# Performance work log

Measured on AMD Instinct MI355X. Metric: run time of the kernel, lower is better.

The kernel has to match this reference:

```python
import jax, jax.numpy as jnp
import numpy as np
from jax import lax

B, CIN, H, W = 32, 256, 28, 28
COUT, KS, KEXP = 256, 3, 4
HIDDEN = int(CIN * 0.25)  # ratio hard-coded to 0.25 in the module


def setup_inputs() -> dict:
    key = jax.random.key(0)
    k1, k2, k3, k4 = jax.random.split(key, 4)
    x = jax.random.normal(k1, (B, CIN, H, W), dtype=jnp.float32)
    # SE (InvertedEx) params: fc1 (1x1 conv, no bias), fc2 (1x1 conv, bias)
    fc1_w = jax.random.normal(k2, (HIDDEN, CIN), dtype=jnp.float32) * np.float32(np.sqrt(2.0 / CIN))
    fc2_w = jax.random.normal(k3, (KEXP * COUT, HIDDEN), dtype=jnp.float32) * np.float32(np.sqrt(2.0 / HIDDEN))
    fc2_b = jnp.zeros((KEXP * COUT,), dtype=jnp.float32)
    # K expert conv kernels, he_std = sqrt(2) * (CIN*KS^2)^-0.5
    he_std = np.float32(np.sqrt(2.0) * (CIN * KS * KS) ** -0.5)
    weight = jax.random.normal(k4, (KEXP, COUT, CIN, KS, KS), dtype=jnp.float32) * he_std
    return {"x": x, "fc1_w": fc1_w, "fc2_w": fc2_w, "fc2_b": fc2_b, "weight": weight}


def reference(x, fc1_w, fc2_w, fc2_b, weight):
    # --- SE routing ---
    pooled = jnp.mean(x, axis=(2, 3))                        # [B, CIN]
    h = jax.nn.relu(pooled @ fc1_w.T)                        # [B, HIDDEN]
    y = (h @ fc2_w.T + fc2_b).reshape(B, KEXP, COUT)         # [B, K, COUT]
    prob = jax.nn.softmax(y / jnp.sqrt(jnp.float32(HIDDEN)), axis=1)  # softmax over K
    # --- aggregate per-sample kernels ---
    agg_w = jnp.einsum('bko,koihw->boihw', prob, weight)     # [B, COUT, CIN, KS, KS]
    # --- per-sample conv (batched implicit GEMM via vmap) ---
    def conv1(xi, wi):
        return lax.conv_general_dilated(
            xi[None], wi, window_strides=(1, 1), padding=((1, 1), (1, 1)),
            dimension_numbers=('NCHW', 'OIHW', 'NCHW'))[0]
    out = jax.vmap(conv1)(x, agg_w)                          # [B, COUT, H, W]
    return out
```

## Files before the change

### kernel.cpp

```cpp
#include <hip/hip_runtime.h>
#include <math.h>

#define B_    32
#define CIN_  256
#define HW_   784
#define H_    28
#define W_    28
#define COUT_ 256
#define KEXP_ 4
#define HID_  64

typedef short short8 __attribute__((ext_vector_type(8)));
typedef unsigned short ushort4v __attribute__((ext_vector_type(4)));
typedef float floatx16 __attribute__((ext_vector_type(16)));

__device__ __forceinline__ unsigned short f2bf(float f) {
    union { float f; unsigned int u; } v; v.f = f;
    unsigned int r = (v.u + 0x7FFFu + ((v.u >> 16) & 1u)) >> 16;
    return (unsigned short)r;
}

__global__ __launch_bounds__(256) void xpose_pool_kernel(const float* __restrict__ x,
                                                         unsigned short* __restrict__ x_t,
                                                         float* __restrict__ partial) {
    __shared__ float tile[32][33];
    int bid = blockIdx.x;
    int b   = bid / 200;
    int rem = bid - b * 200;
    int icg = rem / 25;
    int pxt = rem % 25;
    int ic0 = icg * 32;
    int px0 = pxt * 32;
    int t = threadIdx.x;
    int c = t & 31, rr = t >> 5;
    #pragma unroll
    for (int r = 0; r < 4; ++r) {
        int icr = rr + r * 8;
        int px = px0 + c;
        float v = (px < HW_) ? x[((size_t)(b * CIN_ + ic0 + icr)) * HW_ + px] : 0.f;
        tile[icr][c] = v;
    }
    __syncthreads();
    #pragma unroll
    for (int r = 0; r < 4; ++r) {
        int pxr = rr + r * 8;
        int px = px0 + pxr;
        if (px < HW_)
            x_t[((size_t)b * HW_ + px) * CIN_ + ic0 + c] = f2bf(tile[c][pxr]);
    }
    if (t < 32) {
        float s = 0.f;
        #pragma unroll
        for (int cc = 0; cc < 32; ++cc) s += tile[t][cc];
        partial[((size_t)b * 25 + pxt) * CIN_ + ic0 + t] = s * (1.0f / HW_);
    }
}

__global__ __launch_bounds__(256) void pool_kernel(const float* __restrict__ x,
                                                   float* __restrict__ pooled) {
    int w = blockIdx.x * 4 + (threadIdx.x >> 6);
    int lane = threadIdx.x & 63;
    const float* p = x + (size_t)w * HW_;
    float s = 0.f;
    for (int i = lane; i < HW_; i += 64) s += p[i];
    for (int off = 32; off; off >>= 1) s += __shfl_down(s, off);
    if (lane == 0) pooled[w] = s * (1.0f / HW_);
}

__global__ __launch_bounds__(256) void se3_kernel(const float* __restrict__ partial,
                                                  const float* __restrict__ fc1_w,
                                                  const float* __restrict__ fc2_w,
                                                  const float* __restrict__ fc2_b,
                                                  float* __restrict__ prob) {
    __shared__ float pl[CIN_];
    __shared__ float h[HID_];
    __shared__ float wb[16640];
    int b = blockIdx.x, t = threadIdx.x;
    {
        float s = 0.f;
        for (int pt = 0; pt < 25; ++pt)
            s += partial[((size_t)b * 25 + pt) * CIN_ + t];
        pl[t] = s;
    }
    #pragma unroll
    for (int i = 0; i < 16; ++i) {
        int l = t + i * 256;
        float4 v = *(const float4*)(fc1_w + (size_t)l * 4);
        int r = l >> 6, cc = (l & 63) * 4;
        float* dst = &wb[r * 257 + cc];
        dst[0] = v.x; dst[1] = v.y; dst[2] = v.z; dst[3] = v.w;
    }
    __syncthreads();
    if (t < HID_) {
        float s = 0.f;
        const float* wr = &wb[t * 257];
        for (int c = 0; c < CIN_; ++c) s += pl[c] * wr[c];
        h[t] = fmaxf(s, 0.f);
    }
    float yk[KEXP_];
    for (int k = 0; k < KEXP_; ++k) {
        __syncthreads();
        #pragma unroll
        for (int i = 0; i < 16; ++i) {
            int l = t + i * 256;
            float4 v = *(const float4*)(fc2_w + (size_t)k * COUT_ * HID_ + (size_t)l * 4);
            int o = l >> 4, jj = (l & 15) * 4;
            float* dst = &wb[o * 65 + jj];
            dst[0] = v.x; dst[1] = v.y; dst[2] = v.z; dst[3] = v.w;
        }
        __syncthreads();
        float s = fc2_b[k * COUT_ + t];
        const float* wr = &wb[t * 65];
        #pragma unroll
        for (int j = 0; j < HID_; ++j) s += h[j] * wr[j];
        yk[k] = s * 0.125f;
    }
    float m = yk[0];
    for (int k = 1; k < KEXP_; ++k) m = fmaxf(m, yk[k]);
    float e[KEXP_], sum = 0.f;
    for (int k = 0; k < KEXP_; ++k) { e[k] = expf(yk[k] - m); sum += e[k]; }
    float inv = 1.0f / sum;
    for (int k = 0; k < KEXP_; ++k)
        prob[b * (KEXP_ * COUT_) + k * COUT_ + t] = e[k] * inv;
}

__global__ __launch_bounds__(256) void se2_kernel(const float* __restrict__ pooled,
                                                  const float* __restrict__ fc1_w,
                                                  const float* __restrict__ fc2_w,
                                                  const float* __restrict__ fc2_b,
                                                  float* __restrict__ prob) {
    __shared__ float pl[CIN_];
    __shared__ float h[HID_];
    __shared__ float wb[16640];
    int b = blockIdx.x, t = threadIdx.x;
    pl[t] = pooled[b * CIN_ + t];
    #pragma unroll
    for (int i = 0; i < 16; ++i) {
        int l = t + i * 256;
        float4 v = *(const float4*)(fc1_w + (size_t)l * 4);
        int r = l >> 6, cc = (l & 63) * 4;
        float* dst = &wb[r * 257 + cc];
        dst[0] = v.x; dst[1] = v.y; dst[2] = v.z; dst[3] = v.w;
    }
    __syncthreads();
    if (t < HID_) {
        float s = 0.f;
        const float* wr = &wb[t * 257];
        for (int c = 0; c < CIN_; ++c) s += pl[c] * wr[c];
        h[t] = fmaxf(s, 0.f);
    }
    float yk[KEXP_];
    for (int k = 0; k < KEXP_; ++k) {
        __syncthreads();
        #pragma unroll
        for (int i = 0; i < 16; ++i) {
            int l = t + i * 256;
            float4 v = *(const float4*)(fc2_w + (size_t)k * COUT_ * HID_ + (size_t)l * 4);
            int o = l >> 4, jj = (l & 15) * 4;
            float* dst = &wb[o * 65 + jj];
            dst[0] = v.x; dst[1] = v.y; dst[2] = v.z; dst[3] = v.w;
        }
        __syncthreads();
        float s = fc2_b[k * COUT_ + t];
        const float* wr = &wb[t * 65];
        #pragma unroll
        for (int j = 0; j < HID_; ++j) s += h[j] * wr[j];
        yk[k] = s * 0.125f;
    }
    float m = yk[0];
    for (int k = 1; k < KEXP_; ++k) m = fmaxf(m, yk[k]);
    float e[KEXP_], sum = 0.f;
    for (int k = 0; k < KEXP_; ++k) { e[k] = expf(yk[k] - m); sum += e[k]; }
    float inv = 1.0f / sum;
    for (int k = 0; k < KEXP_; ++k)
        prob[b * (KEXP_ * COUT_) + k * COUT_ + t] = e[k] * inv;
}

__global__ __launch_bounds__(256) void agg3_kernel(const float* __restrict__ weight,
                                                   const float* __restrict__ prob,
                                                   unsigned short* __restrict__ agg) {
    __shared__ float ws_w[KEXP_ * CIN_ * 9];
    __shared__ float pb[KEXP_][8];
    int bid = blockIdx.x;
    int oc = bid & 255;
    int b0 = (bid >> 8) * 8;
    int t = threadIdx.x;
    #pragma unroll
    for (int i = 0; i < 9; ++i) {
        int e4 = t + i * 256;
        int k = e4 / 576;
        int r4 = e4 - k * 576;
        float4 v = *(const float4*)(weight + (size_t)k * 589824 + (size_t)oc * 2304 + (size_t)r4 * 4);
        *(float4*)&ws_w[e4 * 4] = v;
    }
    if (t < KEXP_ * 8) {
        int k = t >> 3, bb = t & 7;
        pb[k][bb] = prob[(size_t)(b0 + bb) * (KEXP_ * COUT_) + k * COUT_ + oc];
    }
    __syncthreads();
    int icg = t & 63, blane = t >> 6;
    for (int rs = 0; rs < 9; ++rs) {
        float wv[4][4];
        #pragma unroll
        for (int q = 0; q < 4; ++q)
            #pragma unroll
            for (int k = 0; k < 4; ++k)
                wv[q][k] = ws_w[k * 2304 + (icg * 4 + q) * 9 + rs];
        #pragma unroll
        for (int bb = 0; bb < 2; ++bb) {
            int bidx = blane * 2 + bb;
            float p0 = pb[0][bidx], p1 = pb[1][bidx], p2 = pb[2][bidx], p3 = pb[3][bidx];
            ushort4v pack;
            #pragma unroll
            for (int q = 0; q < 4; ++q) {
                float s = p0 * wv[q][0] + p1 * wv[q][1] + p2 * wv[q][2] + p3 * wv[q][3];
                pack[q] = f2bf(s);
            }
            *(ushort4v*)(agg + ((((size_t)(b0 + bidx) * 9 + rs) * COUT_ + oc)) * CIN_ + icg * 4) = pack;
        }
    }
}

__global__ __launch_bounds__(256, 1) void conv_mfma3_kernel(const unsigned short* __restrict__ x_t,
                                                            const unsigned short* __restrict__ agg,
                                                            float* __restrict__ out) {
    __shared__ __align__(16) short Xs[2][9 * 35 * 72];

    int gid = blockIdx.x;
    int b      = gid & 31;
    int oc0    = ((gid >> 5) & 1) * 128;
    int rowblk = gid >> 6;
    int py0 = rowblk * 7;

    int t = threadIdx.x;
    int lane = t & 63, w = t >> 6;
    int ml = lane & 31, kh = lane >> 5;

    floatx16 acc[7];
    #pragma unroll
    for (int j = 0; j < 7; ++j)
        #pragma unroll
        for (int r = 0; r < 16; ++r) acc[j][r] = 0.f;

    const unsigned short* xtb = x_t + (size_t)b * HW_ * CIN_;
    const unsigned short* aln = agg + (((size_t)b * 9 * COUT_) + oc0 + w * 32 + ml) * CIN_ + kh * 8;

    {
        #pragma unroll
        for (int i = 0; i < 10; ++i) {
            int l = t + i * 256;
            if (l < 2520) {
                int pos = l >> 3, g = l & 7;
                int row = pos / 35, col = pos - row * 35;
                int gy = py0 - 1 + row, gx = col - 1;
                short8 v = (short8)0;
                if ((unsigned)gy < 28u && (unsigned)gx < 28u)
                    v = *(const short8*)(xtb + ((size_t)(gy * W_ + gx)) * CIN_ + g * 8);
                *(short8*)&Xs[0][pos * 72 + g * 8] = v;
            }
        }
    }

    short8 Acur0, Acur1, Acur2, Anext0, Anext1, Anext2;
    Acur0 = *(const short8*)(aln + (size_t)(0 * 3 + 0) * (COUT_ * CIN_));
    Acur1 = *(const short8*)(aln + (size_t)(1 * 3 + 0) * (COUT_ * CIN_));
    Acur2 = *(const short8*)(aln + (size_t)(2 * 3 + 0) * (COUT_ * CIN_));
    int dxn = 1, kkn = 0, icn = 0;

    __syncthreads();

    for (int c = 0; c < 4; ++c) {
        int ic0 = c * 64;
        const short* xb = &Xs[c & 1][0];

        short8 Xl[10];
        if (c < 3) {
            #pragma unroll
            for (int i = 0; i < 10; ++i) {
                int l = t + i * 256;
                short8 v = (short8)0;
                if (l < 2520) {
                    int pos = l >> 3, g = l & 7;
                    int row = pos / 35, col = pos - row * 35;
                    int gy = py0 - 1 + row, gx = col - 1;
                    if ((unsigned)gy < 28u && (unsigned)gx < 28u)
                        v = *(const short8*)(xtb + ((size_t)(gy * W_ + gx)) * CIN_ + ic0 + 64 + g * 8);
                }
                Xl[i] = v;
            }
        }

        for (int kk = 0; kk < 4; ++kk) {
            for (int dx = 0; dx < 3; ++dx) {
                if (icn < 256) {
                    const unsigned short* ap = aln + icn + kkn * 16;
                    Anext0 = *(const short8*)(ap + (size_t)(0 * 3 + dxn) * (COUT_ * CIN_));
                    Anext1 = *(const short8*)(ap + (size_t)(1 * 3 + dxn) * (COUT_ * CIN_));
                    Anext2 = *(const short8*)(ap + (size_t)(2 * 3 + dxn) * (COUT_ * CIN_));
                    ++dxn;
                    if (dxn == 3) { dxn = 0; ++kkn; if (kkn == 4) { kkn = 0; icn += 64; } }
                }
                int va = (ml + dx) * 72 + kk * 16 + kh * 8;
                #pragma unroll
                for (int r = 0; r < 9; ++r) {
                    short8 Bf = *(const short8*)&xb[r * 2520 + va];
                    if (r <= 6)
                        acc[r]     = __builtin_amdgcn_mfma_f32_32x32x16_bf16(Acur0, Bf, acc[r], 0, 0, 0);
                    if (r >= 1 && r - 1 <= 6)
                        acc[r - 1] = __builtin_amdgcn_mfma_f32_32x32x16_bf16(Acur1, Bf, acc[r - 1], 0, 0, 0);
                    if (r >= 2)
                        acc[r - 2] = __builtin_amdgcn_mfma_f32_32x32x16_bf16(Acur2, Bf, acc[r - 2], 0, 0, 0);
                }
                Acur0 = Anext0; Acur1 = Anext1; Acur2 = Anext2;
            }
        }

        if (c < 3) {
            short* dstb = &Xs[(c & 1) ^ 1][0];
            #pragma unroll
            for (int i = 0; i < 10; ++i) {
                int l = t + i * 256;
                if (l < 2520) {
                    int pos = l >> 3, g = l & 7;
                    *(short8*)&dstb[pos * 72 + g * 8] = Xl[i];
                }
            }
        }
        __syncthreads();
    }

    if (ml < W_) {
        #pragma unroll
        for (int j = 0; j < 7; ++j) {
            float* op = out + ((size_t)(b * COUT_ + oc0 + w * 32)) * HW_ + (py0 + j) * W_ + ml;
            #pragma unroll
            for (int r = 0; r < 16; ++r) {
                int ocd = (r & 3) + 8 * (r >> 2) + 4 * kh;
                op[(size_t)ocd * HW_] = acc[j][r];
            }
        }
    }
}

__global__ __launch_bounds__(256) void conv_kernel(const float* __restrict__ x,
                                                   const float* __restrict__ weight,
                                                   const float* __restrict__ prob,
                                                   float* __restrict__ out) {
    __shared__ float xs[30 * 30];
    __shared__ float wagg[8][32][12];
    __shared__ float pl[KEXP_][8];

    int b  = blockIdx.x >> 5;
    int o0 = (blockIdx.x & 31) * 8;
    int t  = threadIdx.x;

    if (t < 32) {
        int k = t >> 3, oc = t & 7;
        pl[k][oc] = prob[b * (KEXP_ * COUT_) + k * COUT_ + o0 + oc];
    }
    int p0 = t;
    int pr[4], pc[4];
    bool pv[4];
    #pragma unroll
    for (int j = 0; j < 4; ++j) {
        int p = p0 + j * 256;
        pv[j] = p < HW_;
        pr[j] = p / W_;
        pc[j] = p % W_;
    }
    float acc[8][4];
    #pragma unroll
    for (int oc = 0; oc < 8; ++oc)
        #pragma unroll
        for (int j = 0; j < 4; ++j) acc[oc][j] = 0.f;

    int aoc = t >> 5, aii = t & 31;

    for (int ic0 = 0; ic0 < CIN_; ic0 += 32) {
        __syncthreads();
        {
            float w9[9];
            #pragma unroll
            for (int j = 0; j < 9; ++j) w9[j] = 0.f;
            int i = ic0 + aii;
            #pragma unroll
            for (int k = 0; k < KEXP_; ++k) {
                float pk = pl[k][aoc];
                const float* wp = weight + ((size_t)(k * COUT_ + o0 + aoc) * CIN_ + i) * 9;
                #pragma unroll
                for (int j = 0; j < 9; ++j) w9[j] += pk * wp[j];
            }
            #pragma unroll
            for (int j = 0; j < 9; ++j) wagg[aoc][aii][j] = w9[j];
        }
        for (int ii = 0; ii < 32; ++ii) {
            int i = ic0 + ii;
            __syncthreads();
            const float* xp = x + (size_t)(b * CIN_ + i) * HW_;
            for (int e = t; e < 900; e += 256) {
                int ry = e / 30, cx = e - ry * 30;
                int gy = ry - 1, gx = cx - 1;
                float v = 0.f;
                if ((unsigned)gy < 28u && (unsigned)gx < 28u) v = xp[gy * W_ + gx];
                xs[e] = v;
            }
            __syncthreads();
            float xv[4][9];
            #pragma unroll
            for (int j = 0; j < 4; ++j) {
                if (pv[j]) {
                    const float* xr = &xs[pr[j] * 30 + pc[j]];
                    xv[j][0] = xr[0];  xv[j][1] = xr[1];  xv[j][2] = xr[2];
                    xv[j][3] = xr[30]; xv[j][4] = xr[31]; xv[j][5] = xr[32];
                    xv[j][6] = xr[60]; xv[j][7] = xr[61]; xv[j][8] = xr[62];
                } else {
                    #pragma unroll
                    for (int q = 0; q < 9; ++q) xv[j][q] = 0.f;
                }
            }
            #pragma unroll
            for (int oc = 0; oc < 8; ++oc) {
                float4 wa = *(const float4*)&wagg[oc][ii][0];
                float4 wb2 = *(const float4*)&wagg[oc][ii][4];
                float  wc = wagg[oc][ii][8];
                #pragma unroll
                for (int j = 0; j < 4; ++j) {
                    acc[oc][j] += xv[j][0] * wa.x + xv[j][1] * wa.y + xv[j][2] * wa.z
                                + xv[j][3] * wa.w + xv[j][4] * wb2.x + xv[j][5] * wb2.y
                                + xv[j][6] * wb2.z + xv[j][7] * wb2.w + xv[j][8] * wc;
                }
            }
        }
    }
    #pragma unroll
    for (int oc = 0; oc < 8; ++oc) {
        float* op = out + (size_t)(b * COUT_ + o0 + oc) * HW_ + p0;
        #pragma unroll
        for (int j = 0; j < 4; ++j)
            if (pv[j]) op[j * 256] = acc[oc][j];
    }
}

extern "C" void kernel_launch(void* const* d_in, const int* in_sizes, int n_in,
                              void* d_out, int out_size, void* d_ws, size_t ws_size,
                              hipStream_t stream) {
    const float* x     = (const float*)d_in[0];
    const float* fc1_w = (const float*)d_in[1];
    const float* fc2_w = (const float*)d_in[2];
    const float* fc2_b = (const float*)d_in[3];
    const float* weight= (const float*)d_in[4];
    float* out = (float*)d_out;

    char* ws = (char*)d_ws;
    float* prob = (float*)(ws);
    unsigned short* x_t = (unsigned short*)(ws + 131072);
    unsigned short* agg = (unsigned short*)(ws + 12976128);
    float* partial = (float*)(ws + 12976128);
    const size_t WS_NEED = 12976128 + (size_t)B_ * 9 * COUT_ * CIN_ * 2;

    if (ws_size >= WS_NEED) {
        xpose_pool_kernel<<<B_ * 8 * 25, 256, 0, stream>>>(x, x_t, partial);
        se3_kernel<<<B_, 256, 0, stream>>>(partial, fc1_w, fc2_w, fc2_b, prob);
        agg3_kernel<<<4 * COUT_, 256, 0, stream>>>(weight, prob, agg);
        conv_mfma3_kernel<<<256, 256, 0, stream>>>(x_t, agg, out);
    } else {
        float* pooled = (float*)(ws + 131072);
        pool_kernel<<<(B_ * CIN_) / 4, 256, 0, stream>>>(x, pooled);
        se2_kernel<<<B_, 256, 0, stream>>>(pooled, fc1_w, fc2_w, fc2_b, prob);
        conv_kernel<<<B_ * (COUT_ / 8), 256, 0, stream>>>(x, weight, prob, out);
    }
}
```

Baseline: 149.3 us.

## Store aggregated kernels in MFMA fragment order and retile aggregation kernel

The per-sample aggregated weights are now written in a layout matching the MFMA A-fragment order: each (batch, ic-chunk, kk, rs, oc-group) block is 512 contiguous bf16 values, so each lane's short8 load in the conv kernel is contiguous across the wave instead of strided by CIN. The aggregation kernel is retiled to 256 blocks, each covering 32 output channels, 16 input channels and 16 batches. Each block stages its weight slice in padded LDS and writes 16-byte packed stores. This targets uncoalesced A-operand global loads in the conv and the scattered small stores in aggregation, at the cost of fewer aggregation blocks and a more complex index mapping.

```diff
diff --git a/kernel.cpp b/kernel.cpp
--- a/kernel.cpp
+++ b/kernel.cpp
@@ -12,6 +12,7 @@
 
 typedef short short8 __attribute__((ext_vector_type(8)));
 typedef unsigned short ushort4v __attribute__((ext_vector_type(4)));
+typedef unsigned short ushort8v __attribute__((ext_vector_type(8)));
 typedef float floatx16 __attribute__((ext_vector_type(16)));
 
 __device__ __forceinline__ unsigned short f2bf(float f) {
@@ -176,47 +177,63 @@
         prob[b * (KEXP_ * COUT_) + k * COUT_ + t] = e[k] * inv;
 }
 
-__global__ __launch_bounds__(256) void agg3_kernel(const float* __restrict__ weight,
+__global__ __launch_bounds__(256) void agg4_kernel(const float* __restrict__ weight,
                                                    const float* __restrict__ prob,
                                                    unsigned short* __restrict__ agg) {
-    __shared__ float ws_w[KEXP_ * CIN_ * 9];
-    __shared__ float pb[KEXP_][8];
-    int bid = blockIdx.x;
-    int oc = bid & 255;
-    int b0 = (bid >> 8) * 8;
+    __shared__ float wlds[4][32][145];
+    int gid = blockIdx.x;
+    int og  = gid & 7;
+    int icc = (gid >> 3) & 3;
+    int kk  = (gid >> 5) & 3;
+    int bh  = gid >> 7;
+    int oc0 = og * 32;
+    int ic0 = icc * 64 + kk * 16;
     int t = threadIdx.x;
-    #pragma unroll
-    for (int i = 0; i < 9; ++i) {
-        int e4 = t + i * 256;
-        int k = e4 / 576;
-        int r4 = e4 - k * 576;
-        float4 v = *(const float4*)(weight + (size_t)k * 589824 + (size_t)oc * 2304 + (size_t)r4 * 4);
-        *(float4*)&ws_w[e4 * 4] = v;
-    }
-    if (t < KEXP_ * 8) {
-        int k = t >> 3, bb = t & 7;
-        pb[k][bb] = prob[(size_t)(b0 + bb) * (KEXP_ * COUT_) + k * COUT_ + oc];
+
+    #pragma unroll
+    for (int i = 0; i < 18; ++i) {
+        int idx = t + i * 256;
+        int k  = idx / 1152;
+        int r  = idx - k * 1152;
+        int oc = r / 36;
+        int f4 = r - oc * 36;
+        float4 v = *(const float4*)(weight + ((size_t)(k * COUT_ + oc0 + oc) * CIN_ + ic0) * 9 + f4 * 4);
+        float* dst = &wlds[k][oc][f4 * 4];
+        dst[0] = v.x; dst[1] = v.y; dst[2] = v.z; dst[3] = v.w;
+    }
+
+    int lane = t & 63, wv = t >> 6;
+    int ml = lane & 31, kh = lane >> 5;
+
+    float pbr[4][4];
+    #pragma unroll
+    for (int bi = 0; bi < 4; ++bi) {
+        int b = bh * 16 + wv * 4 + bi;
+        #pragma unroll
+        for (int k = 0; k < 4; ++k)
+            pbr[bi][k] = prob[(size_t)b * (KEXP_ * COUT_) + k * COUT_ + oc0 + ml];
     }
     __syncthreads();
-    int icg = t & 63, blane = t >> 6;
+
     for (int rs = 0; rs < 9; ++rs) {
-        float wv[4][4];
-        #pragma unroll
-        for (int q = 0; q < 4; ++q)
-            #pragma unroll
-            for (int k = 0; k < 4; ++k)
-                wv[q][k] = ws_w[k * 2304 + (icg * 4 + q) * 9 + rs];
-        #pragma unroll
-        for (int bb = 0; bb < 2; ++bb) {
-            int bidx = blane * 2 + bb;
-            float p0 = pb[0][bidx], p1 = pb[1][bidx], p2 = pb[2][bidx], p3 = pb[3][bidx];
-            ushort4v pack;
-            #pragma unroll
-            for (int q = 0; q < 4; ++q) {
-                float s = p0 * wv[q][0] + p1 * wv[q][1] + p2 * wv[q][2] + p3 * wv[q][3];
-                pack[q] = f2bf(s);
-            }
-            *(ushort4v*)(agg + ((((size_t)(b0 + bidx) * 9 + rs) * COUT_ + oc)) * CIN_ + icg * 4) = pack;
+        float wreg[4][8];
+        #pragma unroll
+        for (int k = 0; k < 4; ++k)
+            #pragma unroll
+            for (int j = 0; j < 8; ++j)
+                wreg[k][j] = wlds[k][ml][(kh * 8 + j) * 9 + rs];
+        #pragma unroll
+        for (int bi = 0; bi < 4; ++bi) {
+            int b = bh * 16 + wv * 4 + bi;
+            ushort8v pack;
+            #pragma unroll
+            for (int j = 0; j < 8; ++j) {
+                float s = pbr[bi][0] * wreg[0][j] + pbr[bi][1] * wreg[1][j]
+                        + pbr[bi][2] * wreg[2][j] + pbr[bi][3] * wreg[3][j];
+                pack[j] = f2bf(s);
+            }
+            *(ushort8v*)(agg + (size_t)(b * 16 + icc * 4 + kk) * 36864
+                             + (size_t)rs * 4096 + og * 512 + lane * 8) = pack;
         }
     }
 }
@@ -228,13 +245,15 @@
 
     int gid = blockIdx.x;
     int b      = gid & 31;
-    int oc0    = ((gid >> 5) & 1) * 128;
+    int half   = (gid >> 5) & 1;
+    int oc0    = half * 128;
     int rowblk = gid >> 6;
     int py0 = rowblk * 7;
 
     int t = threadIdx.x;
     int lane = t & 63, w = t >> 6;
     int ml = lane & 31, kh = lane >> 5;
+    int og = half * 4 + w;
 
     floatx16 acc[7];
     #pragma unroll
@@ -243,7 +262,7 @@
         for (int r = 0; r < 16; ++r) acc[j][r] = 0.f;
 
     const unsigned short* xtb = x_t + (size_t)b * HW_ * CIN_;
-    const unsigned short* aln = agg + (((size_t)b * 9 * COUT_) + oc0 + w * 32 + ml) * CIN_ + kh * 8;
+    const unsigned short* aln = agg + (size_t)b * 589824 + og * 512 + lane * 8;
 
     {
         #pragma unroll
@@ -262,9 +281,9 @@
     }
 
     short8 Acur0, Acur1, Acur2, Anext0, Anext1, Anext2;
-    Acur0 = *(const short8*)(aln + (size_t)(0 * 3 + 0) * (COUT_ * CIN_));
-    Acur1 = *(const short8*)(aln + (size_t)(1 * 3 + 0) * (COUT_ * CIN_));
-    Acur2 = *(const short8*)(aln + (size_t)(2 * 3 + 0) * (COUT_ * CIN_));
+    Acur0 = *(const short8*)(aln);
+    Acur1 = *(const short8*)(aln + 12288);
+    Acur2 = *(const short8*)(aln + 24576);
     int dxn = 1, kkn = 0, icn = 0;
 
     __syncthreads();
@@ -293,10 +312,11 @@
         for (int kk = 0; kk < 4; ++kk) {
             for (int dx = 0; dx < 3; ++dx) {
                 if (icn < 256) {
-                    const unsigned short* ap = aln + icn + kkn * 16;
-                    Anext0 = *(const short8*)(ap + (size_t)(0 * 3 + dxn) * (COUT_ * CIN_));
-                    Anext1 = *(const short8*)(ap + (size_t)(1 * 3 + dxn) * (COUT_ * CIN_));
-                    Anext2 = *(const short8*)(ap + (size_t)(2 * 3 + dxn) * (COUT_ * CIN_));
+                    const unsigned short* ap = aln + (size_t)(icn >> 6) * 147456
+                                                   + (size_t)kkn * 36864 + (size_t)dxn * 4096;
+                    Anext0 = *(const short8*)(ap);
+                    Anext1 = *(const short8*)(ap + 12288);
+                    Anext2 = *(const short8*)(ap + 24576);
                     ++dxn;
                     if (dxn == 3) { dxn = 0; ++kkn; if (kkn == 4) { kkn = 0; icn += 64; } }
                 }
@@ -461,7 +481,7 @@
     if (ws_size >= WS_NEED) {
         xpose_pool_kernel<<<B_ * 8 * 25, 256, 0, stream>>>(x, x_t, partial);
         se3_kernel<<<B_, 256, 0, stream>>>(partial, fc1_w, fc2_w, fc2_b, prob);
-        agg3_kernel<<<4 * COUT_, 256, 0, stream>>>(weight, prob, agg);
+        agg4_kernel<<<256, 256, 0, stream>>>(weight, prob, agg);
         conv_mfma3_kernel<<<256, 256, 0, stream>>>(x_t, agg, out);
     } else {
         float* pooled = (float*)(ws + 131072);
```

Measured after the change: 149.2 us. Within noise of the previous version (-0.1%).
